# Optimization experiments

Hardware: AMD Instinct MI355X
Metric: run time of the kernel (lower is better)

The kernel has to match this reference:

```python
import jax, jax.numpy as jnp
import numpy as np

DIM = 768
HEADS = 12
HEAD_DIM = DIM // HEADS
NUM_CLASSES = 1000
SCALE = HEAD_DIM ** (-0.5)


def setup_inputs() -> dict:
    key = jax.random.key(0)
    ks = jax.random.split(key, 6)
    B, N = 4, 2048
    s = 0.02
    return {
        "x": jax.random.normal(ks[0], (B, N, DIM), dtype=jnp.float32),
        "w_qkv": jax.random.normal(ks[1], (DIM, 3 * DIM), dtype=jnp.float32) * s,
        "w_proj": jax.random.normal(ks[2], (DIM, DIM), dtype=jnp.float32) * s,
        "b_proj": jax.random.normal(ks[3], (DIM,), dtype=jnp.float32) * s,
        "w_head": jax.random.normal(ks[4], (DIM, NUM_CLASSES), dtype=jnp.float32) * s,
        "b_head": jax.random.normal(ks[5], (NUM_CLASSES,), dtype=jnp.float32) * s,
    }


def reference(x, w_qkv, w_proj, b_proj, w_head, b_head):
    B, N, C = x.shape
    qkv = (x @ w_qkv).reshape(B, N, 3, HEADS, HEAD_DIM)
    qkv = jnp.transpose(qkv, (2, 0, 3, 1, 4))  # [3, B, H, N, hd]
    q, k, v = qkv[0], qkv[1], qkv[2]
    attn = jnp.einsum("bhnd,bhmd->bhnm", q, k) * SCALE  # [B,H,N,N]
    attn = jax.nn.softmax(attn, axis=-1)
    out = jnp.einsum("bhnm,bhmd->bhnd", attn, v)  # [B,H,N,hd]
    out = jnp.transpose(out, (0, 2, 1, 3)).reshape(B, N, C)
    out = out @ w_proj + b_proj
    out = out @ w_head + b_head  # [B,N,num_classes]
    return jnp.max(out, axis=1)  # [B,num_classes]
```

## Files before the change

kernel.cpp:

```cpp
#include <hip/hip_runtime.h>
#include <hip/hip_bf16.h>

typedef __attribute__((ext_vector_type(8))) short short8;
typedef __attribute__((ext_vector_type(4))) float f32x4;
typedef __attribute__((ext_vector_type(16))) float f32x16;
typedef unsigned short u16t;
typedef unsigned int u32t;

#define MFMA16(a, b, c) __builtin_amdgcn_mfma_f32_16x16x32_bf16((a), (b), (c), 0, 0, 0)
#define MFMA32(a, b, c) __builtin_amdgcn_mfma_f32_32x32x16_bf16((a), (b), (c), 0, 0, 0)

__device__ __forceinline__ u16t f2b(float f) {
    union { float f; u32t u; } v; v.f = f;
    u32t u = v.u + 0x7FFFu + ((v.u >> 16) & 1u);
    return (u16t)(u >> 16);
}
__device__ __forceinline__ u32t encf(float f) {
    union { float f; u32t u; } v; v.f = f;
    return (v.u & 0x80000000u) ? ~v.u : (v.u | 0x80000000u);
}
__device__ __forceinline__ float decf(u32t u) {
    union { u32t u; float f; } v;
    v.u = (u & 0x80000000u) ? (u ^ 0x80000000u) : ~u;
    return v.f;
}
__device__ __forceinline__ float fexp2(float x) {
#if __has_builtin(__builtin_amdgcn_exp2f)
    return __builtin_amdgcn_exp2f(x);
#else
    return __expf(x * 0.6931471805599453f);
#endif
}
__device__ __forceinline__ void gload16(const u16t* g, u16t* l) {
    __builtin_amdgcn_global_load_lds((const __attribute__((address_space(1))) void*)g,
                                     (__attribute__((address_space(3))) void*)l, 16, 0, 0);
}

__global__ __launch_bounds__(256) void k_cast_x(const float* __restrict__ x, u16t* __restrict__ xb) {
    int i = blockIdx.x * 256 + threadIdx.x;
    float4 v = ((const float4*)x)[i];
    ushort4 o;
    o.x = f2b(v.x); o.y = f2b(v.y); o.z = f2b(v.z); o.w = f2b(v.w);
    ((ushort4*)xb)[i] = o;
}

__global__ __launch_bounds__(256) void k_transpose(const float* __restrict__ W, u16t* __restrict__ WT,
                                                   int K, int N, int NP) {
    __shared__ float t[32][33];
    int n0 = blockIdx.x * 32, k0 = blockIdx.y * 32;
    int tx = threadIdx.x, ty = threadIdx.y;
    for (int i = 0; i < 32; i += 8) {
        int k = k0 + ty + i, n = n0 + tx;
        t[ty + i][tx] = (n < N) ? W[(size_t)k * N + n] : 0.f;
    }
    __syncthreads();
    for (int i = 0; i < 32; i += 8) {
        int n = n0 + ty + i, k = k0 + tx;
        if (n < NP) WT[(size_t)n * K + k] = f2b(t[tx][ty + i]);
    }
}

__global__ __launch_bounds__(256) void k_bias_f(const float* __restrict__ bproj, const float* __restrict__ whead,
                                                const float* __restrict__ bhead, float* __restrict__ bf) {
    __shared__ float red[256];
    int t = threadIdx.x;
    int c = t & 15;
    int jg = t >> 4;
    int n = blockIdx.x * 16 + c;
    float s = 0.f;
    if (n < 1000) {
#pragma unroll 4
        for (int j = jg * 48; j < jg * 48 + 48; ++j)
            s += bproj[j] * whead[j * 1000 + n];
    }
    red[t] = s;
    __syncthreads();
    for (int off = 128; off >= 16; off >>= 1) {
        if (t < off) red[t] += red[t + off];
        __syncthreads();
    }
    if (t < 16) {
        int nn = blockIdx.x * 16 + t;
        bf[nn] = (nn < 1000) ? (red[t] + bhead[nn]) : 0.f;
    }
}

__global__ __launch_bounds__(256) void k_init_out(u32t* __restrict__ o, int n) {
    int i = blockIdx.x * 256 + threadIdx.x;
    if (i < n) o[i] = 0u;
}
__global__ __launch_bounds__(256) void k_decode_out(u32t* __restrict__ o, int n) {
    int i = blockIdx.x * 256 + threadIdx.x;
    if (i < n) {
        float f = decf(o[i]);
        ((float*)o)[i] = f;
    }
}

#define BM 128
#define BN 128

#define QSCALE 0.18033688011112042f

template <int EPI>
__global__ __launch_bounds__(256) void k_gemm_bt(const u16t* __restrict__ A, const u16t* __restrict__ BT,
                                                 int M, int N, int K,
                                                 u16t* __restrict__ Cb, const float* __restrict__ bias,
                                                 u32t* __restrict__ omax) {
    __shared__ alignas(16) u16t As[BM * 64];
    __shared__ alignas(16) u16t Bs[BN * 64];
    int tid = threadIdx.x;
    int lane = tid & 63, wid = tid >> 6;
    int wr = wid >> 1, wc = wid & 1;
    int g = lane >> 4, l15 = lane & 15;
    int m0 = blockIdx.y * BM, n0 = blockIdx.x * BN;

    f32x4 acc[4][4];
    for (int i = 0; i < 4; i++)
        for (int j = 0; j < 4; j++) acc[i][j] = (f32x4){0.f, 0.f, 0.f, 0.f};

    const u16t* pa[4]; const u16t* pb[4]; u16t* da[4]; u16t* db[4];
#pragma unroll
    for (int i = 0; i < 4; i++) {
        int c = tid + 256 * i;
        int row = (c >> 2) & 127;
        int kcol = (c >> 9) * 32 + (c & 3) * 8;
        pa[i] = A + (size_t)(m0 + row) * K + kcol;
        pb[i] = BT + (size_t)(n0 + row) * K + kcol;
        da[i] = &As[c * 8];
        db[i] = &Bs[c * 8];
    }

    for (int k0 = 0; k0 < K; k0 += 64) {
#pragma unroll
        for (int i = 0; i < 4; i++) gload16(pa[i] + k0, da[i]);
#pragma unroll
        for (int i = 0; i < 4; i++) gload16(pb[i] + k0, db[i]);
        __syncthreads();
#pragma unroll
        for (int kk = 0; kk < 2; kk++) {
            short8 af[4], bf[4];
#pragma unroll
            for (int i = 0; i < 4; i++) af[i] = *(const short8*)&As[kk * 4096 + (wr * 64 + i * 16 + l15) * 32 + g * 8];
#pragma unroll
            for (int j = 0; j < 4; j++) bf[j] = *(const short8*)&Bs[kk * 4096 + (wc * 64 + j * 16 + l15) * 32 + g * 8];
#pragma unroll
            for (int i = 0; i < 4; i++)
#pragma unroll
                for (int j = 0; j < 4; j++) acc[i][j] = MFMA16(af[i], bf[j], acc[i][j]);
        }
        __syncthreads();
    }

    if constexpr (EPI == 0) {
        for (int i = 0; i < 4; i++)
            for (int j = 0; j < 4; j++)
                for (int r = 0; r < 4; r++) {
                    int row = m0 + wr * 64 + i * 16 + g * 4 + r;
                    int col = n0 + wc * 64 + j * 16 + l15;
                    int t = col / 768, rem = col - t * 768;
                    int hh = rem >> 6, d = rem & 63;
                    int bb = row >> 11, n = row & 2047;
                    float v = acc[i][j][r];
                    size_t idx;
                    if (t == 0) {
                        v *= QSCALE;
                        idx = ((size_t)(bb * 12 + hh)) * 131072 + (size_t)n * 64 + d;
                    } else if (t == 1) {
                        idx = ((size_t)(48 + bb * 12 + hh)) * 131072 + (size_t)n * 64 + d;
                    } else {
                        int np = (n & ~12) | ((n & 4) << 1) | ((n & 8) >> 1);
                        idx = ((size_t)(96 + bb * 12 + hh)) * 131072 + (size_t)d * 2048 + np;
                    }
                    Cb[idx] = f2b(v);
                }
    } else if constexpr (EPI == 1) {
        for (int i = 0; i < 4; i++)
            for (int j = 0; j < 4; j++)
                for (int r = 0; r < 4; r++) {
                    int row = m0 + wr * 64 + i * 16 + g * 4 + r;
                    int col = n0 + wc * 64 + j * 16 + l15;
                    Cb[(size_t)row * N + col] = f2b(acc[i][j][r] + bias[col]);
                }
    } else if constexpr (EPI == 3) {
        for (int i = 0; i < 4; i++)
            for (int j = 0; j < 4; j++)
                for (int r = 0; r < 4; r++) {
                    int row = m0 + wr * 64 + i * 16 + g * 4 + r;
                    int col = n0 + wc * 64 + j * 16 + l15;
                    Cb[(size_t)row * N + col] = f2b(acc[i][j][r]);
                }
    } else {
        __shared__ float smax[2][BN];
        float cmax[4];
        for (int j = 0; j < 4; j++) {
            float m = -3.0e38f;
            for (int i = 0; i < 4; i++)
                for (int r = 0; r < 4; r++) m = fmaxf(m, acc[i][j][r]);
            m = fmaxf(m, __shfl_xor(m, 16));
            m = fmaxf(m, __shfl_xor(m, 32));
            cmax[j] = m;
        }
        if (lane < 16)
            for (int j = 0; j < 4; j++) smax[wr][wc * 64 + j * 16 + lane] = cmax[j];
        __syncthreads();
        if (tid < BN) {
            int col = n0 + tid;
            if (col < 1000) {
                float m = fmaxf(smax[0][tid], smax[1][tid]) + bias[col];
                int b = m0 >> 11;
                atomicMax(&omax[b * 1000 + col], encf(m));
            }
        }
    }
}

__global__ __launch_bounds__(256) void k_flash(const u16t* __restrict__ QKV, u16t* __restrict__ AO) {
    __shared__ alignas(16) u16t Kc[3][4096];
    __shared__ alignas(16) u16t Vc[3][4096];

    const int tid = threadIdx.x;
    const int lane = tid & 63;
    const int h = lane >> 5;
    const int l31 = lane & 31;
    const int w = tid >> 6;
    const int wk = ((blockIdx.x & 7) * 96) + (blockIdx.x >> 3);
    const int qt = wk & 15;
    const int hb = wk >> 4;
    const int head = hb % 12, b = hb / 12;
    const u16t* Qg = QKV + ((size_t)hb) * 131072;
    const u16t* Kg = QKV + ((size_t)(48 + hb)) * 131072;
    const u16t* Vg = QKV + ((size_t)(96 + hb)) * 131072;
    const int q0w = qt * 128 + w * 32;

    short8 qf[4];
#pragma unroll
    for (int ks = 0; ks < 4; ++ks)
        qf[ks] = *(const short8*)&Qg[(size_t)(q0w + l31) * 64 + ks * 16 + h * 8];
    asm volatile("s_waitcnt vmcnt(0)" ::: "memory");

    short8 vone;
#pragma unroll
    for (int e = 0; e < 8; ++e) vone[e] = (short)0x3F80;

    f32x16 o0, o1, lsum;
#pragma unroll
    for (int r = 0; r < 16; ++r) { o0[r] = 0.f; o1[r] = 0.f; lsum[r] = 0.f; }

    auto stage = [&](int bi, int kv0) {
#pragma unroll
        for (int c = 0; c < 2; ++c) {
            int ic = c * 256 + tid;
            int ss = ic >> 8, ks = (ic >> 6) & 3, l6 = ic & 63;
            int hh = l6 >> 5, lq = l6 & 31;
            const u16t* gs = Kg + ((size_t)(kv0 + ss * 32 + lq) << 6) + ks * 16 + hh * 8;
            gload16(gs, &Kc[bi][ic * 8]);
        }
#pragma unroll
        for (int c = 0; c < 2; ++c) {
            int ic = c * 256 + tid;
            int jb = ic >> 8, ks = (ic >> 6) & 3, l6 = ic & 63;
            int hh = l6 >> 5, ld = l6 & 31;
            const u16t* gs = Vg + (size_t)(jb * 32 + ld) * 2048 + kv0 + ks * 16 + hh * 8;
            gload16(gs, &Vc[bi][ic * 8]);
        }
    };

    stage(0, 0);
    stage(1, 64);

#pragma unroll 1
    for (int t = 0; t < 32; ++t) {
        const int cur = t % 3;
        if (t < 30) {
            stage((t + 2) % 3, (t + 2) * 64);
            asm volatile("s_waitcnt vmcnt(8)" ::: "memory");
        } else if (t == 30) {
            asm volatile("s_waitcnt vmcnt(4)" ::: "memory");
        } else {
            asm volatile("s_waitcnt vmcnt(0)" ::: "memory");
        }
        __builtin_amdgcn_s_barrier();

        const u16t* Kb = &Kc[cur][0];
        const u16t* Vb = &Vc[cur][0];

        f32x16 s0, s1;
#pragma unroll
        for (int r = 0; r < 16; ++r) { s0[r] = 0.f; s1[r] = 0.f; }
        __builtin_amdgcn_s_setprio(1);
#pragma unroll
        for (int ks = 0; ks < 4; ++ks) {
            short8 k0 = *(const short8*)&Kb[(ks * 64 + lane) * 8];
            short8 k1 = *(const short8*)&Kb[((4 + ks) * 64 + lane) * 8];
            s0 = MFMA32(k0, qf[ks], s0);
            s1 = MFMA32(k1, qf[ks], s1);
        }
        __builtin_amdgcn_s_setprio(0);

        short8 pf[4];
        auto packhalf = [&](const f32x16& sv, int half, int idx) {
            union { u32t wu[4]; short8 v; } u;
#pragma unroll
            for (int wq = 0; wq < 4; ++wq) {
                float lo = fexp2(sv[half * 8 + 2 * wq]);
                float hi = fexp2(sv[half * 8 + 2 * wq + 1]);
                asm("v_cvt_pk_bf16_f32 %0, %1, %2" : "=v"(u.wu[wq]) : "v"(lo), "v"(hi));
            }
            pf[idx] = u.v;
        };
        packhalf(s0, 0, 0);
        packhalf(s0, 1, 1);
        packhalf(s1, 0, 2);
        packhalf(s1, 1, 3);

        __builtin_amdgcn_s_setprio(1);
#pragma unroll
        for (int ks = 0; ks < 4; ++ks) {
            short8 v0 = *(const short8*)&Vb[(ks * 64 + lane) * 8];
            short8 v1 = *(const short8*)&Vb[((4 + ks) * 64 + lane) * 8];
            o0 = MFMA32(pf[ks], v0, o0);
            o1 = MFMA32(pf[ks], v1, o1);
            lsum = MFMA32(pf[ks], vone, lsum);
        }
        __builtin_amdgcn_s_setprio(0);

        asm volatile("s_waitcnt lgkmcnt(0)" ::: "memory");
        __builtin_amdgcn_s_barrier();
    }

#pragma unroll
    for (int r = 0; r < 16; ++r) {
        int q = (r & 3) + 8 * (r >> 2) + 4 * h;
        float rn = 1.0f / lsum[r];
        u16t* dst = AO + (size_t)(b * 2048 + q0w + q) * 768 + head * 64;
        dst[l31] = f2b(o0[r] * rn);
        dst[32 + l31] = f2b(o1[r] * rn);
    }
}

extern "C" void kernel_launch(void* const* d_in, const int* in_sizes, int n_in,
                              void* d_out, int out_size, void* d_ws, size_t ws_size,
                              hipStream_t stream) {
    const float* x = (const float*)d_in[0];
    const float* w_qkv = (const float*)d_in[1];
    const float* w_proj = (const float*)d_in[2];
    const float* b_proj = (const float*)d_in[3];
    const float* w_head = (const float*)d_in[4];
    const float* b_head = (const float*)d_in[5];

    char* ws = (char*)d_ws;
    u16t* xb = (u16t*)(ws);
    u16t* wqkvT = (u16t*)(ws + 12582912);
    u16t* wheadT = (u16t*)(ws + 16121856);
    u16t* wprojb = (u16t*)(ws + 17694720);
    u16t* qkv = (u16t*)(ws + 18874368);
    u16t* ao = (u16t*)(ws + 56623104);
    u16t* WfT = (u16t*)(ws + 69206016);
    float* bias_f = (float*)(ws + 70778880);

    dim3 tb(32, 8);
    k_cast_x<<<6144, 256, 0, stream>>>(x, xb);
    k_cast_x<<<576, 256, 0, stream>>>(w_proj, (u16t*)wprojb);
    k_transpose<<<dim3(2304 / 32, 768 / 32), tb, 0, stream>>>(w_qkv, wqkvT, 768, 2304, 2304);
    k_transpose<<<dim3(1024 / 32, 768 / 32), tb, 0, stream>>>(w_head, wheadT, 768, 1000, 1024);
    k_init_out<<<16, 256, 0, stream>>>((u32t*)d_out, 4000);
    k_bias_f<<<64, 256, 0, stream>>>(b_proj, w_head, b_head, bias_f);

    k_gemm_bt<3><<<dim3(768 / 128, 1024 / 128), 256, 0, stream>>>(wheadT, wprojb, 1024, 768, 768, WfT, nullptr, nullptr);

    k_gemm_bt<0><<<dim3(2304 / 128, 8192 / 128), 256, 0, stream>>>(xb, wqkvT, 8192, 2304, 768, qkv, nullptr, nullptr);
    k_flash<<<768, 256, 0, stream>>>(qkv, ao);
    k_gemm_bt<2><<<dim3(1024 / 128, 8192 / 128), 256, 0, stream>>>(ao, WfT, 8192, 1024, 768, nullptr, bias_f, (u32t*)d_out);

    k_decode_out<<<16, 256, 0, stream>>>((u32t*)d_out, 4000);
}
```

Before: 210.1 us.

## Double-buffer GEMM shared-memory tiles to overlap global loads with MFMA

Turns the bf16 GEMM main loop into a two-stage pipeline. The next K-tile is loaded into a second LDS buffer while MFMAs run on the current one, with explicit vmcnt waits and raw barriers in place of __syncthreads. The aim is to hide global-to-LDS load latency in the QKV, projection and head GEMMs. It doubles LDS use, which may reduce occupancy, and adds a barrier before the max-reduction epilogue.

```diff
diff --git a/kernel.cpp b/kernel.cpp
--- a/kernel.cpp
+++ b/kernel.cpp
@@ -107,8 +107,8 @@
                                                  int M, int N, int K,
                                                  u16t* __restrict__ Cb, const float* __restrict__ bias,
                                                  u32t* __restrict__ omax) {
-    __shared__ alignas(16) u16t As[BM * 64];
-    __shared__ alignas(16) u16t Bs[BN * 64];
+    __shared__ alignas(16) u16t As[2][BM * 64];
+    __shared__ alignas(16) u16t Bs[2][BN * 64];
     int tid = threadIdx.x;
     int lane = tid & 63, wid = tid >> 6;
     int wr = wid >> 1, wc = wid & 1;
@@ -127,29 +127,48 @@
         int kcol = (c >> 9) * 32 + (c & 3) * 8;
         pa[i] = A + (size_t)(m0 + row) * K + kcol;
         pb[i] = BT + (size_t)(n0 + row) * K + kcol;
-        da[i] = &As[c * 8];
-        db[i] = &Bs[c * 8];
-    }
-
-    for (int k0 = 0; k0 < K; k0 += 64) {
-#pragma unroll
-        for (int i = 0; i < 4; i++) gload16(pa[i] + k0, da[i]);
-#pragma unroll
-        for (int i = 0; i < 4; i++) gload16(pb[i] + k0, db[i]);
-        __syncthreads();
+        da[i] = &As[0][c * 8];
+        db[i] = &Bs[0][c * 8];
+    }
+
+    auto stage = [&](int buf, int k0) {
+        int boff = buf * (BM * 64);
+#pragma unroll
+        for (int i = 0; i < 4; i++) gload16(pa[i] + k0, da[i] + boff);
+#pragma unroll
+        for (int i = 0; i < 4; i++) gload16(pb[i] + k0, db[i] + boff);
+    };
+
+    const int NT = K >> 6;
+    stage(0, 0);
+
+#pragma unroll 1
+    for (int t = 0; t < NT; ++t) {
+        const int cur = t & 1;
+        if (t + 1 < NT) {
+            stage(cur ^ 1, (t + 1) << 6);
+            asm volatile("s_waitcnt vmcnt(8)" ::: "memory");
+        } else {
+            asm volatile("s_waitcnt vmcnt(0)" ::: "memory");
+        }
+        __builtin_amdgcn_s_barrier();
+
+        const u16t* Ab = &As[cur][0];
+        const u16t* Bb = &Bs[cur][0];
 #pragma unroll
         for (int kk = 0; kk < 2; kk++) {
             short8 af[4], bf[4];
 #pragma unroll
-            for (int i = 0; i < 4; i++) af[i] = *(const short8*)&As[kk * 4096 + (wr * 64 + i * 16 + l15) * 32 + g * 8];
-#pragma unroll
-            for (int j = 0; j < 4; j++) bf[j] = *(const short8*)&Bs[kk * 4096 + (wc * 64 + j * 16 + l15) * 32 + g * 8];
+            for (int i = 0; i < 4; i++) af[i] = *(const short8*)&Ab[kk * 4096 + (wr * 64 + i * 16 + l15) * 32 + g * 8];
+#pragma unroll
+            for (int j = 0; j < 4; j++) bf[j] = *(const short8*)&Bb[kk * 4096 + (wc * 64 + j * 16 + l15) * 32 + g * 8];
 #pragma unroll
             for (int i = 0; i < 4; i++)
 #pragma unroll
                 for (int j = 0; j < 4; j++) acc[i][j] = MFMA16(af[i], bf[j], acc[i][j]);
         }
-        __syncthreads();
+        asm volatile("s_waitcnt lgkmcnt(0)" ::: "memory");
+        __builtin_amdgcn_s_barrier();
     }
 
     if constexpr (EPI == 0) {
@@ -201,6 +220,7 @@
             m = fmaxf(m, __shfl_xor(m, 32));
             cmax[j] = m;
         }
+        __syncthreads();
         if (lane < 16)
             for (int j = 0; j < 4; j++) smax[wr][wc * 64 + j * 16 + lane] = cmax[j];
         __syncthreads();
```

Measured after the change: 202.4 us. -3.7%, faster.
